# Optimization experiments

Hardware: AMD Instinct MI355X
Metric: run time of the kernel (lower is better)

The kernel has to match this reference:

```python
import jax, jax.numpy as jnp
import numpy as np

N, M, K = 262144, 65536, 32
C_IN, C_OUT = 64, 128
BN_EPS = 1e-5


def setup_inputs() -> dict:
    key = jax.random.key(0)
    ks = jax.random.split(key, 6)
    p = jax.random.normal(ks[0], (N, 3), jnp.float32)
    x = jax.random.normal(ks[1], (N, C_IN), jnp.float32)
    o = jnp.array([N], jnp.int32)  # single-cloud batch offsets
    idx = jnp.sort(jax.random.randint(ks[2], (M,), 0, N))  # sampled point indices (FPS stand-in)
    knn_idx = jax.random.randint(ks[3], (M, K), 0, N)      # neighbor indices (ball-query/knn stand-in)
    # learned params: Linear(C_IN+3 -> C_OUT) + BatchNorm1d(C_OUT)
    W = jax.random.normal(ks[4], (C_IN + 3, C_OUT), jnp.float32) / np.sqrt(C_IN + 3).astype(np.float32)
    b = jnp.zeros((C_OUT,), jnp.float32)
    gamma = jnp.ones((C_OUT,), jnp.float32)
    beta = jnp.zeros((C_OUT,), jnp.float32)
    return dict(p=p, x=x, o=o, idx=idx, knn_idx=knn_idx, W=W, b=b, gamma=gamma, beta=beta)


def reference(p, x, o, idx, knn_idx, W, b, gamma, beta):
    # sampler: n_p = p[idx]
    n_p = p[idx]  # [M, 3]
    # pooling with with_xyz=True: gather K neighbors, concat relative xyz, max-pool over K
    rel = p[knn_idx] - n_p[:, None, :]                      # [M, K, 3]
    grouped = jnp.concatenate([rel, x[knn_idx]], axis=-1)   # [M, K, 3+C_IN]
    pooled = grouped.max(axis=1)                            # [M, 3+C_IN]
    # convs: Linear -> BatchNorm1d (training-mode batch stats) -> ReLU
    h = pooled @ W + b                                      # [M, C_OUT]
    mean = h.mean(axis=0)
    var = h.var(axis=0)
    h = (h - mean) * jax.lax.rsqrt(var + BN_EPS) * gamma + beta
    x_out = jnp.maximum(h, 0.0)
    n_o = jnp.array([idx.shape[0]], jnp.int32)
    return (n_p, x_out, n_o)
```

## Files before the change

### kernel.cpp

```cpp
#include <hip/hip_runtime.h>
#include <hip/hip_fp16.h>
#include <math.h>

#define K_NB   32
#define C_IN   64
#define C_OUT  128
#define KP     96
#define TILE   128
#define BN_EPS 1e-5f

typedef _Float16 f16x8 __attribute__((ext_vector_type(8)));
typedef float    f32x4 __attribute__((ext_vector_type(4)));
typedef float    f32x2 __attribute__((ext_vector_type(2)));

__device__ __forceinline__ unsigned pk(float a, float b) {
    __half2 h = __floats2half2_rn(a, b);
    return *reinterpret_cast<unsigned*>(&h);
}

__device__ __forceinline__ unsigned pkmax(unsigned a, unsigned b) {
    unsigned d;
    asm volatile("v_pk_max_f16 %0, %1, %2" : "=v"(d) : "v"(a), "v"(b));
    return d;
}

using pkrtz_t = decltype(__builtin_amdgcn_cvt_pkrtz(0.f, 0.f));
__device__ __forceinline__ unsigned h2u(pkrtz_t v) {
    union { pkrtz_t h; unsigned u; } c; c.h = v; return c.u;
}

__device__ __forceinline__ void fp8x4_to_h2x2(unsigned d, unsigned& lo, unsigned& hi) {
    f32x2 a = __builtin_amdgcn_cvt_pk_f32_fp8((int)d, false);
    f32x2 b = __builtin_amdgcn_cvt_pk_f32_fp8((int)d, true);
    lo = h2u(__builtin_amdgcn_cvt_pkrtz(a.x, a.y));
    hi = h2u(__builtin_amdgcn_cvt_pkrtz(b.x, b.y));
}

__global__ __launch_bounds__(256) void sa_zero(float* __restrict__ g, int n)
{
    for (int i = threadIdx.x; i < n; i += 256) g[i] = 0.f;
}

__global__ __launch_bounds__(256) void sa_cvt(
    const float4* __restrict__ x4, uint4* __restrict__ xq, int n16,
    float* __restrict__ gsum, int ng)
{
    if (blockIdx.x == 0)
        for (int i = threadIdx.x; i < ng; i += 256) gsum[i] = 0.f;
    for (int i = blockIdx.x * blockDim.x + threadIdx.x; i < n16;
         i += gridDim.x * blockDim.x) {
        float4 v0 = x4[4*i+0], v1 = x4[4*i+1], v2 = x4[4*i+2], v3 = x4[4*i+3];
        int w0 = 0, w1 = 0, w2 = 0, w3 = 0;
        w0 = __builtin_amdgcn_cvt_pk_fp8_f32(v0.x, v0.y, w0, false);
        w0 = __builtin_amdgcn_cvt_pk_fp8_f32(v0.z, v0.w, w0, true);
        w1 = __builtin_amdgcn_cvt_pk_fp8_f32(v1.x, v1.y, w1, false);
        w1 = __builtin_amdgcn_cvt_pk_fp8_f32(v1.z, v1.w, w1, true);
        w2 = __builtin_amdgcn_cvt_pk_fp8_f32(v2.x, v2.y, w2, false);
        w2 = __builtin_amdgcn_cvt_pk_fp8_f32(v2.z, v2.w, w2, true);
        w3 = __builtin_amdgcn_cvt_pk_fp8_f32(v3.x, v3.y, w3, false);
        w3 = __builtin_amdgcn_cvt_pk_fp8_f32(v3.z, v3.w, w3, true);
        xq[i] = make_uint4((unsigned)w0, (unsigned)w1, (unsigned)w2, (unsigned)w3);
    }
}

__global__ __launch_bounds__(256) void sa_pool_h(
    const float* __restrict__ p, const uint2* __restrict__ xq2,
    const int* __restrict__ idx, const int* __restrict__ knn,
    float* __restrict__ np_out, float* __restrict__ hbuf)
{
    const int lane = threadIdx.x & 63;
    const int m    = blockIdx.x * 4 + (threadIdx.x >> 6);

    int kidx = 0;
    if (lane < K_NB) kidx = knn[m * K_NB + lane];

    unsigned mx0 = 0xFC00FC00u, mx1 = 0xFC00FC00u;
    unsigned mx2 = 0xFC00FC00u, mx3 = 0xFC00FC00u;

    const int sub = lane & 7;
    #pragma unroll
    for (int i = 0; i < 4; ++i) {
        int nb = __shfl(kidx, i * 8 + (lane >> 3));
        uint2 u = xq2[(size_t)nb * 8 + sub];
        unsigned h01, h23, h45, h67;
        fp8x4_to_h2x2(u.x, h01, h23);
        fp8x4_to_h2x2(u.y, h45, h67);
        mx0 = pkmax(mx0, h01);
        mx1 = pkmax(mx1, h23);
        mx2 = pkmax(mx2, h45);
        mx3 = pkmax(mx3, h67);
    }
    #pragma unroll
    for (int off = 8; off <= 32; off <<= 1) {
        mx0 = pkmax(mx0, (unsigned)__shfl_xor((int)mx0, off));
        mx1 = pkmax(mx1, (unsigned)__shfl_xor((int)mx1, off));
        mx2 = pkmax(mx2, (unsigned)__shfl_xor((int)mx2, off));
        mx3 = pkmax(mx3, (unsigned)__shfl_xor((int)mx3, off));
    }

    float px = -INFINITY, py = -INFINITY, pz = -INFINITY;
    if (lane < K_NB) {
        const float* pp = p + (size_t)kidx * 3;
        px = pp[0]; py = pp[1]; pz = pp[2];
    }
    #pragma unroll
    for (int off = 32; off >= 1; off >>= 1) {
        px = fmaxf(px, __shfl_xor(px, off));
        py = fmaxf(py, __shfl_xor(py, off));
        pz = fmaxf(pz, __shfl_xor(pz, off));
    }

    const int s = idx[m];
    const float npx = p[(size_t)s*3+0];
    const float npy = p[(size_t)s*3+1];
    const float npz = p[(size_t)s*3+2];
    if (lane < 3) np_out[(size_t)m*3 + lane] = (lane == 0) ? npx : (lane == 1 ? npy : npz);

    const int tile = m >> 7, rl = m & (TILE - 1);
    __half* rowh = (__half*)(hbuf + (size_t)tile * TILE * C_OUT) + rl * KP;
    if (lane < 8) {
        *(uint4*)(rowh + lane * 8) = make_uint4(mx0, mx1, mx2, mx3);
    } else if (lane == 8) {
        *(uint4*)(rowh + 64) = make_uint4(pk(px-npx, py-npy), pk(pz-npz, 0.f), 0u, 0u);
    } else if (lane < 12) {
        *(uint4*)(rowh + 64 + (lane - 8) * 8) = make_uint4(0u, 0u, 0u, 0u);
    }
}

__global__ __launch_bounds__(256) void sa_pool_f(
    const float* __restrict__ p, const float* __restrict__ x,
    const int* __restrict__ idx, const int* __restrict__ knn,
    float* __restrict__ np_out, float* __restrict__ hbuf)
{
    const int lane = threadIdx.x & 63;
    const int m    = blockIdx.x * 4 + (threadIdx.x >> 6);
    int kidx = 0;
    if (lane < K_NB) kidx = knn[m * K_NB + lane];
    float xmax = -INFINITY;
    #pragma unroll
    for (int k = 0; k < K_NB; ++k) {
        int nb = __shfl(kidx, k);
        xmax = fmaxf(xmax, x[(size_t)nb * C_IN + lane]);
    }
    float px = -INFINITY, py = -INFINITY, pz = -INFINITY;
    if (lane < K_NB) {
        const float* pp = p + (size_t)kidx * 3;
        px = pp[0]; py = pp[1]; pz = pp[2];
    }
    #pragma unroll
    for (int off = 32; off >= 1; off >>= 1) {
        px = fmaxf(px, __shfl_xor(px, off));
        py = fmaxf(py, __shfl_xor(py, off));
        pz = fmaxf(pz, __shfl_xor(pz, off));
    }
    const int s = idx[m];
    const float npx = p[(size_t)s*3], npy = p[(size_t)s*3+1], npz = p[(size_t)s*3+2];
    if (lane < 3) np_out[(size_t)m*3 + lane] = (lane == 0) ? npx : (lane == 1 ? npy : npz);

    const int tile = m >> 7, rl = m & (TILE - 1);
    __half* rowh = (__half*)(hbuf + (size_t)tile * TILE * C_OUT) + rl * KP;
    if (lane < 8) {
        float v[8];
        #pragma unroll
        for (int j = 0; j < 8; ++j) v[j] = __shfl(xmax, lane * 8 + j);
        *(uint4*)(rowh + lane * 8) =
            make_uint4(pk(v[0],v[1]), pk(v[2],v[3]), pk(v[4],v[5]), pk(v[6],v[7]));
    } else if (lane == 8) {
        *(uint4*)(rowh + 64) = make_uint4(pk(px-npx, py-npy), pk(pz-npz, 0.f), 0u, 0u);
    } else if (lane < 12) {
        *(uint4*)(rowh + 64 + (lane - 8) * 8) = make_uint4(0u, 0u, 0u, 0u);
    }
}

__global__ __launch_bounds__(256) void sa_gemm_mfma(
    const float* __restrict__ W, const float* __restrict__ bias,
    float* __restrict__ h, float* __restrict__ gsum, unsigned rep_mask)
{
    __shared__ __half Wt[C_OUT][128];
    __shared__ float reds[16][C_OUT];
    __shared__ float redq[16][C_OUT];

    const int t    = threadIdx.x;
    const int wave = t >> 6, lane = t & 63;
    const int l15  = lane & 15, lg = lane >> 4;
    const int m0   = blockIdx.x * TILE;

    for (int e = t; e < C_OUT * KP; e += 256) {
        const int c = e & 127, kk = e >> 7;
        float w = 0.f;
        if (kk < C_IN)          w = W[(size_t)(3 + kk) * C_OUT + c];
        else if (kk < C_IN + 3) w = W[(size_t)(kk - C_IN) * C_OUT + c];
        Wt[c][(((kk >> 3) ^ (c & 7)) << 3) | (kk & 7)] = __float2half(w);
    }

    const __half* tb = (const __half*)(h + (size_t)blockIdx.x * TILE * C_OUT);
    f16x8 A[2][3];
    #pragma unroll
    for (int rt = 0; rt < 2; ++rt) {
        const int rl = wave * 32 + rt * 16 + l15;
        #pragma unroll
        for (int ks = 0; ks < 3; ++ks)
            A[rt][ks] = *(const f16x8*)(tb + (size_t)rl * KP + ks * 32 + lg * 8);
    }
    __syncthreads();

    f32x4 acc[2][8];
    #pragma unroll
    for (int ct = 0; ct < 8; ++ct) {
        const float bc = bias[ct * 16 + l15];
        acc[0][ct] = (f32x4){bc, bc, bc, bc};
        acc[1][ct] = (f32x4){bc, bc, bc, bc};
    }
    #pragma unroll
    for (int ks = 0; ks < 3; ++ks) {
        #pragma unroll
        for (int ct = 0; ct < 8; ++ct) {
            const int c  = ct * 16 + l15;
            const int kc = ks * 4 + lg;
            const f16x8 wf = *(const f16x8*)&Wt[c][((kc ^ (c & 7)) << 3)];
            acc[0][ct] = __builtin_amdgcn_mfma_f32_16x16x32_f16(A[0][ks], wf, acc[0][ct], 0, 0, 0);
            acc[1][ct] = __builtin_amdgcn_mfma_f32_16x16x32_f16(A[1][ks], wf, acc[1][ct], 0, 0, 0);
        }
    }

    float s8[8], q8[8];
    #pragma unroll
    for (int ct = 0; ct < 8; ++ct) { s8[ct] = 0.f; q8[ct] = 0.f; }
    #pragma unroll
    for (int rt = 0; rt < 2; ++rt) {
        #pragma unroll
        for (int ct = 0; ct < 8; ++ct) {
            const int col = ct * 16 + l15;
            #pragma unroll
            for (int r = 0; r < 4; ++r) {
                const int row = m0 + wave * 32 + rt * 16 + lg * 4 + r;
                const float v = acc[rt][ct][r];
                h[(size_t)row * C_OUT + col] = v;
                s8[ct] += v;
                q8[ct]  = fmaf(v, v, q8[ct]);
            }
        }
    }
    #pragma unroll
    for (int ct = 0; ct < 8; ++ct) {
        reds[wave * 4 + lg][ct * 16 + l15] = s8[ct];
        redq[wave * 4 + lg][ct * 16 + l15] = q8[ct];
    }
    __syncthreads();
    if (t < C_OUT) {
        float ss = 0.f, qq = 0.f;
        #pragma unroll
        for (int i = 0; i < 16; ++i) { ss += reds[i][t]; qq += redq[i][t]; }
        float* g = gsum + (size_t)(blockIdx.x & rep_mask) * 2 * C_OUT;
        atomicAdd(&g[t],         ss);
        atomicAdd(&g[C_OUT + t], qq);
    }
}

__global__ __launch_bounds__(256) void sa_bnrelu_fin(
    float* __restrict__ h, const float* __restrict__ gsum,
    const float* __restrict__ gamma, const float* __restrict__ beta,
    float* __restrict__ no_out, int M, int rep)
{
    __shared__ float sc[C_OUT], sh[C_OUT];
    const int t = threadIdx.x;
    if (t < C_OUT) {
        float s = 0.f, s2 = 0.f;
        for (int r = 0; r < rep; ++r) {
            s  += gsum[(size_t)r * 2 * C_OUT + t];
            s2 += gsum[(size_t)r * 2 * C_OUT + C_OUT + t];
        }
        const float inv_m = 1.0f / (float)M;
        const float mean = s * inv_m;
        const float var  = fmaf(-mean, mean, s2 * inv_m);
        const float scv  = gamma[t] * rsqrtf(var + BN_EPS);
        sc[t] = scv;
        sh[t] = fmaf(-mean, scv, beta[t]);
    }
    if (blockIdx.x == 0 && t == 0) no_out[0] = (float)M;
    __syncthreads();

    const size_t total4 = (size_t)M * C_OUT / 4;
    float4* h4 = (float4*)h;
    for (size_t i = (size_t)blockIdx.x * blockDim.x + t;
         i < total4; i += (size_t)gridDim.x * blockDim.x) {
        float4 v = h4[i];
        const int c = (int)((i * 4) & (C_OUT - 1));
        v.x = fmaxf(fmaf(v.x, sc[c+0], sh[c+0]), 0.f);
        v.y = fmaxf(fmaf(v.y, sc[c+1], sh[c+1]), 0.f);
        v.z = fmaxf(fmaf(v.z, sc[c+2], sh[c+2]), 0.f);
        v.w = fmaxf(fmaf(v.w, sc[c+3], sh[c+3]), 0.f);
        h4[i] = v;
    }
}

extern "C" void kernel_launch(void* const* d_in, const int* in_sizes, int n_in,
                              void* d_out, int out_size, void* d_ws, size_t ws_size,
                              hipStream_t stream)
{
    const float* p     = (const float*)d_in[0];
    const float* x     = (const float*)d_in[1];
    const int*   idx   = (const int*)d_in[3];
    const int*   knn   = (const int*)d_in[4];
    const float* W     = (const float*)d_in[5];
    const float* bias  = (const float*)d_in[6];
    const float* gamma = (const float*)d_in[7];
    const float* beta  = (const float*)d_in[8];

    const int N = in_sizes[1] / C_IN;
    const int M = in_sizes[3];

    float* out    = (float*)d_out;
    float* np_out = out;
    float* h      = out + (size_t)M * 3;
    float* no_out = out + (size_t)M * 3 + (size_t)M * C_OUT;

    const size_t xq_bytes = (size_t)N * C_IN;
    const bool   fp8_path = ws_size >= xq_bytes + 2048;

    const size_t tail = fp8_path ? (ws_size - xq_bytes) : ws_size;
    int rep = 1;
    while (rep < 8 && (size_t)(2 * rep) * 2 * C_OUT * sizeof(float) <= tail)
        rep <<= 1;

    float* gsum = fp8_path ? (float*)((char*)d_ws + xq_bytes) : (float*)d_ws;
    const unsigned rep_mask = (unsigned)(rep - 1);

    if (fp8_path) {
        uint4* xq = (uint4*)d_ws;
        const int n16 = N * C_IN / 16;
        sa_cvt   <<<2048, 256, 0, stream>>>((const float4*)x, xq, n16,
                                            gsum, rep * 2 * C_OUT);
        sa_pool_h<<<M / 4, 256, 0, stream>>>(p, (const uint2*)d_ws, idx, knn, np_out, h);
    } else {
        sa_zero  <<<1, 256, 0, stream>>>(gsum, rep * 2 * C_OUT);
        sa_pool_f<<<M / 4, 256, 0, stream>>>(p, x, idx, knn, np_out, h);
    }

    sa_gemm_mfma <<<M / TILE, 256, 0, stream>>>(W, bias, h, gsum, rep_mask);
    sa_bnrelu_fin<<<1024,     256, 0, stream>>>(h, gsum, gamma, beta, no_out, M, rep);
}
```

Baseline: 108.0 us.

## Fuse BatchNorm+ReLU into GEMM kernel via grid-wide atomic barrier

Merges the GEMM and the BN/ReLU kernels into one. Each block reduces its column statistics with wave shuffles, adds them to the global sums atomically, then spins on a global counter until all 512 blocks arrive. After that it computes scale and shift and writes the activated output straight from the accumulators. This removes one full write-then-read-and-write pass over the M×128 fp32 output and one kernel launch. It relies on all blocks being co-resident, since the spin barrier can deadlock otherwise, and it zeroes the counter with the existing reset kernel.

```diff
diff --git a/kernel.cpp b/kernel.cpp
--- a/kernel.cpp
+++ b/kernel.cpp
@@ -172,13 +172,15 @@
     }
 }
 
-__global__ __launch_bounds__(256) void sa_gemm_mfma(
+__global__ __launch_bounds__(256) void sa_gemm_bn(
     const float* __restrict__ W, const float* __restrict__ bias,
-    float* __restrict__ h, float* __restrict__ gsum, unsigned rep_mask)
+    const float* __restrict__ gamma, const float* __restrict__ beta,
+    float* __restrict__ h, float* __restrict__ gsum, unsigned* __restrict__ cnt,
+    float* __restrict__ no_out, unsigned rep_mask, int rep, int M, unsigned nblk)
 {
     __shared__ __half Wt[C_OUT][128];
-    __shared__ float reds[16][C_OUT];
-    __shared__ float redq[16][C_OUT];
+    __shared__ float reds[4][C_OUT];
+    __shared__ float redq[4][C_OUT];
 
     const int t    = threadIdx.x;
     const int wave = t >> 6, lane = t & 63;
@@ -223,74 +225,68 @@
         }
     }
 
-    float s8[8], q8[8];
-    #pragma unroll
-    for (int ct = 0; ct < 8; ++ct) { s8[ct] = 0.f; q8[ct] = 0.f; }
-    #pragma unroll
-    for (int rt = 0; rt < 2; ++rt) {
-        #pragma unroll
-        for (int ct = 0; ct < 8; ++ct) {
-            const int col = ct * 16 + l15;
+    #pragma unroll
+    for (int ct = 0; ct < 8; ++ct) {
+        float s = 0.f, q = 0.f;
+        #pragma unroll
+        for (int rt = 0; rt < 2; ++rt)
             #pragma unroll
             for (int r = 0; r < 4; ++r) {
-                const int row = m0 + wave * 32 + rt * 16 + lg * 4 + r;
                 const float v = acc[rt][ct][r];
-                h[(size_t)row * C_OUT + col] = v;
-                s8[ct] += v;
-                q8[ct]  = fmaf(v, v, q8[ct]);
+                s += v; q = fmaf(v, v, q);
             }
-        }
-    }
-    #pragma unroll
-    for (int ct = 0; ct < 8; ++ct) {
-        reds[wave * 4 + lg][ct * 16 + l15] = s8[ct];
-        redq[wave * 4 + lg][ct * 16 + l15] = q8[ct];
+        s += __shfl_xor(s, 16); s += __shfl_xor(s, 32);
+        q += __shfl_xor(q, 16); q += __shfl_xor(q, 32);
+        if (lg == 0) { reds[wave][ct * 16 + l15] = s; redq[wave][ct * 16 + l15] = q; }
     }
     __syncthreads();
     if (t < C_OUT) {
-        float ss = 0.f, qq = 0.f;
-        #pragma unroll
-        for (int i = 0; i < 16; ++i) { ss += reds[i][t]; qq += redq[i][t]; }
+        const float ss = reds[0][t] + reds[1][t] + reds[2][t] + reds[3][t];
+        const float qq = redq[0][t] + redq[1][t] + redq[2][t] + redq[3][t];
         float* g = gsum + (size_t)(blockIdx.x & rep_mask) * 2 * C_OUT;
         atomicAdd(&g[t],         ss);
         atomicAdd(&g[C_OUT + t], qq);
     }
-}
-
-__global__ __launch_bounds__(256) void sa_bnrelu_fin(
-    float* __restrict__ h, const float* __restrict__ gsum,
-    const float* __restrict__ gamma, const float* __restrict__ beta,
-    float* __restrict__ no_out, int M, int rep)
-{
-    __shared__ float sc[C_OUT], sh[C_OUT];
-    const int t = threadIdx.x;
+    __syncthreads();
+
+    if (t == 0) {
+        __threadfence();
+        __hip_atomic_fetch_add(cnt, 1u, __ATOMIC_RELEASE, __HIP_MEMORY_SCOPE_AGENT);
+        while (__hip_atomic_load(cnt, __ATOMIC_ACQUIRE, __HIP_MEMORY_SCOPE_AGENT) < nblk) {}
+    }
+    __syncthreads();
+
     if (t < C_OUT) {
         float s = 0.f, s2 = 0.f;
         for (int r = 0; r < rep; ++r) {
-            s  += gsum[(size_t)r * 2 * C_OUT + t];
-            s2 += gsum[(size_t)r * 2 * C_OUT + C_OUT + t];
+            s  += __hip_atomic_load(&gsum[(size_t)r * 2 * C_OUT + t],
+                                    __ATOMIC_RELAXED, __HIP_MEMORY_SCOPE_AGENT);
+            s2 += __hip_atomic_load(&gsum[(size_t)r * 2 * C_OUT + C_OUT + t],
+                                    __ATOMIC_RELAXED, __HIP_MEMORY_SCOPE_AGENT);
         }
         const float inv_m = 1.0f / (float)M;
         const float mean = s * inv_m;
         const float var  = fmaf(-mean, mean, s2 * inv_m);
-        const float scv  = gamma[t] * rsqrtf(var + BN_EPS);
-        sc[t] = scv;
-        sh[t] = fmaf(-mean, scv, beta[t]);
+        const float sc   = gamma[t] * rsqrtf(var + BN_EPS);
+        reds[0][t] = sc;
+        redq[0][t] = fmaf(-mean, sc, beta[t]);
     }
     if (blockIdx.x == 0 && t == 0) no_out[0] = (float)M;
     __syncthreads();
 
-    const size_t total4 = (size_t)M * C_OUT / 4;
-    float4* h4 = (float4*)h;
-    for (size_t i = (size_t)blockIdx.x * blockDim.x + t;
-         i < total4; i += (size_t)gridDim.x * blockDim.x) {
-        float4 v = h4[i];
-        const int c = (int)((i * 4) & (C_OUT - 1));
-        v.x = fmaxf(fmaf(v.x, sc[c+0], sh[c+0]), 0.f);
-        v.y = fmaxf(fmaf(v.y, sc[c+1], sh[c+1]), 0.f);
-        v.z = fmaxf(fmaf(v.z, sc[c+2], sh[c+2]), 0.f);
-        v.w = fmaxf(fmaf(v.w, sc[c+3], sh[c+3]), 0.f);
-        h4[i] = v;
+    #pragma unroll
+    for (int rt = 0; rt < 2; ++rt) {
+        #pragma unroll
+        for (int ct = 0; ct < 8; ++ct) {
+            const int col = ct * 16 + l15;
+            const float scv = reds[0][col], shv = redq[0][col];
+            #pragma unroll
+            for (int r = 0; r < 4; ++r) {
+                const int row = m0 + wave * 32 + rt * 16 + lg * 4 + r;
+                h[(size_t)row * C_OUT + col] =
+                    fmaxf(fmaf(acc[rt][ct][r], scv, shv), 0.f);
+            }
+        }
     }
 }
 
@@ -320,23 +316,25 @@
 
     const size_t tail = fp8_path ? (ws_size - xq_bytes) : ws_size;
     int rep = 1;
-    while (rep < 8 && (size_t)(2 * rep) * 2 * C_OUT * sizeof(float) <= tail)
+    while (rep < 8 && (size_t)(2 * rep) * 2 * C_OUT * sizeof(float) + 64 <= tail)
         rep <<= 1;
 
-    float* gsum = fp8_path ? (float*)((char*)d_ws + xq_bytes) : (float*)d_ws;
+    float*    gsum = fp8_path ? (float*)((char*)d_ws + xq_bytes) : (float*)d_ws;
+    unsigned* cnt  = (unsigned*)(gsum + (size_t)rep * 2 * C_OUT);
     const unsigned rep_mask = (unsigned)(rep - 1);
+    const unsigned nblk     = (unsigned)(M / TILE);
 
     if (fp8_path) {
         uint4* xq = (uint4*)d_ws;
         const int n16 = N * C_IN / 16;
         sa_cvt   <<<2048, 256, 0, stream>>>((const float4*)x, xq, n16,
-                                            gsum, rep * 2 * C_OUT);
+                                            gsum, rep * 2 * C_OUT + 1);
         sa_pool_h<<<M / 4, 256, 0, stream>>>(p, (const uint2*)d_ws, idx, knn, np_out, h);
     } else {
-        sa_zero  <<<1, 256, 0, stream>>>(gsum, rep * 2 * C_OUT);
+        sa_zero  <<<1, 256, 0, stream>>>(gsum, rep * 2 * C_OUT + 1);
         sa_pool_f<<<M / 4, 256, 0, stream>>>(p, x, idx, knn, np_out, h);
     }
 
-    sa_gemm_mfma <<<M / TILE, 256, 0, stream>>>(W, bias, h, gsum, rep_mask);
-    sa_bnrelu_fin<<<1024,     256, 0, stream>>>(h, gsum, gamma, beta, no_out, M, rep);
-}
+    sa_gemm_bn<<<nblk, 256, 0, stream>>>(W, bias, gamma, beta, h, gsum, cnt,
+                                         no_out, rep_mask, rep, M, nblk);
+}
```

New measurement: 138.4 us. +28.1%, slower.
